# Kernel optimization log

Hardware: AMD Instinct MI355X
Metric: run time of the kernel (lower is better)

The kernel has to match this reference:

```python
import jax, jax.numpy as jnp
import numpy as np

T, B = 384, 128
IN_DIM, HID, OUT_DIM = 512, 1024, 512


def _lstm_step(h, c, x_t, Wx, Wh, b):
    # x_t: [B, D], h/c: [B, H]; gates order: i, f, g, o
    gates = x_t @ Wx + h @ Wh + b  # [B, 4H]
    i, f, g, o = jnp.split(gates, 4, axis=-1)
    c_new = jax.nn.sigmoid(f) * c + jax.nn.sigmoid(i) * jnp.tanh(g)
    h_new = jax.nn.sigmoid(o) * jnp.tanh(c_new)
    return h_new, c_new


def setup_inputs() -> dict:
    key = jax.random.key(0)
    ks = jax.random.split(key, 9)
    s_in = 1.0 / np.sqrt(IN_DIM)
    s_h = 1.0 / np.sqrt(HID)
    s_o = 1.0 / np.sqrt(OUT_DIM)
    return {
        "x": jax.random.normal(ks[0], (T, B, IN_DIM), dtype=jnp.float32),
        "hidden_state": jnp.zeros((1, B, HID), dtype=jnp.float32),
        "cell_state": jnp.zeros((1, B, HID), dtype=jnp.float32),
        "enc_Wx": jax.random.normal(ks[1], (IN_DIM, 4 * HID), dtype=jnp.float32) * s_in,
        "enc_Wh": jax.random.normal(ks[2], (HID, 4 * HID), dtype=jnp.float32) * s_h,
        "enc_b": jnp.zeros((4 * HID,), dtype=jnp.float32),
        "dec_Wx": jax.random.normal(ks[3], (OUT_DIM, 4 * HID), dtype=jnp.float32) * s_o,
        "dec_Wh": jax.random.normal(ks[4], (HID, 4 * HID), dtype=jnp.float32) * s_h,
        "dec_b": jnp.zeros((4 * HID,), dtype=jnp.float32),
        "fc_W": jax.random.normal(ks[5], (HID, OUT_DIM), dtype=jnp.float32) * s_h,
        "fc_b": jnp.zeros((OUT_DIM,), dtype=jnp.float32),
    }


def reference(x, hidden_state, cell_state, enc_Wx, enc_Wh, enc_b,
              dec_Wx, dec_Wh, dec_b, fc_W, fc_b):
    # ---- encoder: run LSTM over T steps, keep only final hidden state ----
    h0, c0 = hidden_state[0], cell_state[0]  # [B, H]

    def enc_step(carry, x_t):
        h, c = carry
        h, c = _lstm_step(h, c, x_t, enc_Wx, enc_Wh, enc_b)
        return (h, c), None

    (h_enc, _), _ = jax.lax.scan(enc_step, (h0, c0), x)

    y0 = jnp.zeros((B, OUT_DIM), dtype=x.dtype)
    c_dec0 = jnp.zeros((B, HID), dtype=x.dtype)

    def dec_step(carry, _):
        y, h, c = carry
        h, c = _lstm_step(h, c, y, dec_Wx, dec_Wh, dec_b)
        y = jax.nn.softmax(h @ fc_W + fc_b, axis=-1)  # softmax over dim=2
        return (y, h, c), y

    _, output = jax.lax.scan(dec_step, (y0, h_enc, c_dec0), None, length=T)
    return output  # [T, B, OUT_DIM]
```

## Files before the change

### kernel.cpp

```cpp
#include <hip/hip_runtime.h>


#define TS 384

typedef __attribute__((ext_vector_type(8))) short bf16x8;
typedef __attribute__((ext_vector_type(4))) float f32x4;

#define ACT_PLANE 393216u
#define WS_ACT 4096u
#define WS_FP  (WS_ACT + 4u*ACT_PLANE)
#define WS_TOTAL (WS_FP + 2097152u)

__device__ __forceinline__ unsigned short bf16r(float v) {
  unsigned u = __float_as_uint(v);
  u += 0x7FFFu + ((u >> 16) & 1u);
  return (unsigned short)(u >> 16);
}
__device__ __forceinline__ float bf2f(unsigned short h) {
  return __uint_as_float(((unsigned)h) << 16);
}
__device__ __forceinline__ void split2(float v, short& hi, short& lo) {
  unsigned short h = bf16r(v);
  float r = v - bf2f(h);
  hi = (short)h; lo = (short)bf16r(r);
}
__device__ __forceinline__ float sigm(float v)  { return 1.0f / (1.0f + __expf(-v)); }
__device__ __forceinline__ float tanhfa(float v){ return 1.0f - 2.0f / (__expf(2.0f*v) + 1.0f); }

__device__ __forceinline__ void st_u64(short* p, unsigned long long v) {
  __hip_atomic_store((unsigned long long*)p, v, __ATOMIC_RELAXED, __HIP_MEMORY_SCOPE_AGENT);
}
__device__ __forceinline__ void st_f32(float* p, float v) {
  __hip_atomic_store(p, v, __ATOMIC_RELAXED, __HIP_MEMORY_SCOPE_AGENT);
}
__device__ __forceinline__ float ld_f32(const float* p) {
  return __hip_atomic_load(p, __ATOMIC_RELAXED, __HIP_MEMORY_SCOPE_AGENT);
}
__device__ __forceinline__ unsigned ldc(const unsigned* p) {
  return __hip_atomic_load(p, __ATOMIC_RELAXED, __HIP_MEMORY_SCOPE_AGENT);
}

__device__ __forceinline__ int elem_off(int row, int k) {
  int kb = k >> 5, mt = row >> 4, lane = (((k >> 3) & 3) << 4) | (row & 15);
  return (((kb * 8 + mt) * 64) + lane) * 8 + (k & 7);
}

__device__ __forceinline__ void arrive(unsigned* line) {
  asm volatile("s_waitcnt vmcnt(0)" ::: "memory");
  __syncthreads();
  if (threadIdx.x == 0)
    __hip_atomic_fetch_add(line, 1u, __ATOMIC_RELAXED, __HIP_MEMORY_SCOPE_AGENT);
}
__device__ __forceinline__ void wait4(const unsigned* base, unsigned target,
                                      bool fence, int* sDead) {
  if (threadIdx.x == 0) {
    unsigned spins = 0;
    for (;;) {
      unsigned c0 = ldc(base), c1 = ldc(base + 64);
      unsigned c2 = ldc(base + 128), c3 = ldc(base + 192);
      if (c0 >= target && c1 >= target && c2 >= target && c3 >= target) break;
      __builtin_amdgcn_s_sleep(1);
      if (++spins > (1u << 19)) { *sDead = 1; break; }
    }
    if (fence) __builtin_amdgcn_fence(__ATOMIC_ACQUIRE, "agent");
  }
  __syncthreads();
}
__device__ __forceinline__ void wait1(const unsigned* line, unsigned target,
                                      bool fence, int* sDead) {
  if (threadIdx.x == 0) {
    unsigned spins = 0;
    while (ldc(line) < target) {
      __builtin_amdgcn_s_sleep(1);
      if (++spins > (1u << 19)) { *sDead = 1; break; }
    }
    if (fence) __builtin_amdgcn_fence(__ATOMIC_ACQUIRE, "agent");
  }
  __syncthreads();
}

__device__ void load_gate_weights(const float* __restrict__ Wx, const float* __restrict__ Wh,
                                  int p, short* sBh, short* sBl) {
  for (int idx = threadIdx.x; idx < 24576; idx += 1024) {
    int j = idx & 7, l = (idx >> 3) & 63, kb = idx >> 9;
    int k = kb * 32 + ((l >> 4) << 3) + j;
    int c = l & 15;
    int gcol = (c >> 2) * 1024 + p * 4 + (c & 3);
    float wv = (k < 512) ? Wx[(size_t)k * 4096 + gcol]
                         : Wh[(size_t)(k - 512) * 4096 + gcol];
    short hi, lo; split2(wv, hi, lo);
    sBh[idx] = hi; sBl[idx] = lo;
  }
}
__device__ void load_fc_weights(const float* __restrict__ fcW, int kg, int cg,
                                short* sFh, short* sFl) {
  for (int idx = threadIdx.x; idx < 4096; idx += 1024) {
    int j = idx & 7, l = (idx >> 3) & 63, kb = idx >> 9;
    int unit = kg * 256 + kb * 32 + ((l >> 4) << 3) + j;
    int col = cg * 16 + (l & 15);
    short hi, lo; split2(fcW[(size_t)unit * 512 + col], hi, lo);
    sFh[idx] = hi; sFl[idx] = lo;
  }
}

__device__ __forceinline__ void gg_range(
    const bf16x8* __restrict__ AH, const bf16x8* __restrict__ AL,
    const bf16x8* __restrict__ BH, const bf16x8* __restrict__ BL,
    int mt, int l, int kb0, int n2, f32x4* acc)
{
  #pragma unroll 2
  for (int i = 0; i < n2; ++i) {
    int kb = kb0 + i * 2;
    bf16x8 ah0 = AH[(kb * 8 + mt) * 64 + l];
    bf16x8 al0 = AL[(kb * 8 + mt) * 64 + l];
    bf16x8 bh0 = BH[kb * 64 + l];
    bf16x8 bl0 = BL[kb * 64 + l];
    bf16x8 ah1 = AH[((kb + 1) * 8 + mt) * 64 + l];
    bf16x8 al1 = AL[((kb + 1) * 8 + mt) * 64 + l];
    bf16x8 bh1 = BH[(kb + 1) * 64 + l];
    bf16x8 bl1 = BL[(kb + 1) * 64 + l];
    acc[0] = __builtin_amdgcn_mfma_f32_16x16x32_bf16(ah0, bh0, acc[0], 0, 0, 0);
    acc[1] = __builtin_amdgcn_mfma_f32_16x16x32_bf16(ah0, bl0, acc[1], 0, 0, 0);
    acc[2] = __builtin_amdgcn_mfma_f32_16x16x32_bf16(al0, bh0, acc[2], 0, 0, 0);
    acc[3] = __builtin_amdgcn_mfma_f32_16x16x32_bf16(ah1, bh1, acc[3], 0, 0, 0);
    acc[4] = __builtin_amdgcn_mfma_f32_16x16x32_bf16(ah1, bl1, acc[4], 0, 0, 0);
    acc[5] = __builtin_amdgcn_mfma_f32_16x16x32_bf16(al1, bh1, acc[5], 0, 0, 0);
  }
}
__device__ __forceinline__ void gg_finish(f32x4* acc, int kh, int mt, int l,
                                          float* LDSgate) {
  f32x4 s = (acc[0] + acc[3]) + ((acc[1] + acc[4]) + (acc[2] + acc[5]));
  const int col = l & 15, r0 = mt * 16 + ((l >> 4) << 2);
  float* plane = LDSgate + kh * 2176;
  #pragma unroll
  for (int j = 0; j < 4; ++j) plane[(r0 + j) * 17 + col] = s[j];
}

__device__ __forceinline__ void conv_x(const float* __restrict__ xsrc,
                                       short* dstH, short* dstL, int p, int t) {
  if (t < 32) {
    int g = p * 32 + t;
    int l = g & 63, mt = (g >> 6) & 7, kb = g >> 9;
    int row = mt * 16 + (l & 15), k = kb * 32 + ((l >> 4) << 3);
    const float* xs = xsrc + (size_t)row * 512 + k;
    unsigned long long h64[2] = {0, 0}, l64[2] = {0, 0};
    #pragma unroll
    for (int j = 0; j < 8; ++j) {
      short hi, lo; split2(xs[j], hi, lo);
      h64[j >> 2] |= (unsigned long long)(unsigned short)hi << ((j & 3) * 16);
      l64[j >> 2] |= (unsigned long long)(unsigned short)lo << ((j & 3) * 16);
    }
    int off = g * 8;
    st_u64(dstH + off, h64[0]); st_u64(dstH + off + 4, h64[1]);
    st_u64(dstL + off, l64[0]); st_u64(dstL + off + 4, l64[1]);
  }
}

__global__ void __launch_bounds__(1024, 1)
lstm3(const float* __restrict__ x, const float* __restrict__ h0p,
      const float* __restrict__ c0p, const float* __restrict__ eWx,
      const float* __restrict__ eWh, const float* __restrict__ eb,
      const float* __restrict__ dWx, const float* __restrict__ dWh,
      const float* __restrict__ db, const float* __restrict__ fcW,
      const float* __restrict__ fcb, float* __restrict__ out,
      char* __restrict__ ws)
{
  __shared__ __align__(16) short sBh[24576], sBl[24576];
  __shared__ __align__(16) short sFh[4096], sFl[4096];
  __shared__ float LDSgate[2 * 2176];
  __shared__ unsigned hsplit[512];
  __shared__ float ybuf[512];
  __shared__ float red[16];
  __shared__ int sDead;

  const int p = blockIdx.x, t = threadIdx.x;
  const int w = t >> 6, l = t & 63;
  const int mt = w & 7, kh = w >> 3;
  if (t == 0) sDead = 0;

  unsigned* hln = (unsigned*)ws;
  unsigned* yln = (unsigned*)(ws + 1024);
  unsigned* fln = (unsigned*)(ws + 2048);

  float* fp = (float*)(ws + WS_FP);
  short* planeH[2] = { (short*)(ws + WS_ACT),             (short*)(ws + WS_ACT + 2*ACT_PLANE) };
  short* planeL[2] = { (short*)(ws + WS_ACT + ACT_PLANE), (short*)(ws + WS_ACT + 3*ACT_PLANE) };

  const int row_pw = t & 127, u_pw = (t >> 7) & 3;
  unsigned* my_hline = hln + (p >> 6) * 64;

  load_gate_weights(eWx, eWh, p, sBh, sBl);
  conv_x(x, planeH[0], planeL[0], p, t);
  if (t < 64) {
    int g = 8192 + p * 64 + t;
    int ll = g & 63, mtt = (g >> 6) & 7, kb = g >> 9;
    int row = mtt * 16 + (ll & 15), k = kb * 32 + ((ll >> 4) << 3);
    const float* hs = h0p + (size_t)row * 1024 + (k - 512);
    unsigned long long h64[2] = {0, 0}, l64[2] = {0, 0};
    #pragma unroll
    for (int j = 0; j < 8; ++j) {
      short hi, lo; split2(hs[j], hi, lo);
      h64[j >> 2] |= (unsigned long long)(unsigned short)hi << ((j & 3) * 16);
      l64[j >> 2] |= (unsigned long long)(unsigned short)lo << ((j & 3) * 16);
    }
    int off = g * 8;
    st_u64(planeH[0] + off, h64[0]); st_u64(planeH[0] + off + 4, h64[1]);
    st_u64(planeL[0] + off, l64[0]); st_u64(planeL[0] + off + 4, l64[1]);
  }
  float creg = 0.f, bq0 = 0.f, bq1 = 0.f, bq2 = 0.f, bq3 = 0.f;
  if (t < 512) {
    creg = c0p[(size_t)row_pw * 1024 + p * 4 + u_pw];
    bq0 = eb[0 * 1024 + p * 4 + u_pw];
    bq1 = eb[1 * 1024 + p * 4 + u_pw];
    bq2 = eb[2 * 1024 + p * 4 + u_pw];
    bq3 = eb[3 * 1024 + p * 4 + u_pw];
  }
  arrive(my_hline);

  for (int st = 0; st < TS; ++st) {
    int rb = st & 1, wb = rb ^ 1;
    wait4(hln, 64u * (st + 1), true, &sDead);
    if (sDead) return;
    {
      f32x4 z = {0.f, 0.f, 0.f, 0.f};
      f32x4 acc[6] = {z, z, z, z, z, z};
      gg_range((const bf16x8*)planeH[rb], (const bf16x8*)planeL[rb],
               (const bf16x8*)sBh, (const bf16x8*)sBl, mt, l, kh * 24, 12, acc);
      gg_finish(acc, kh, mt, l, LDSgate);
    }
    __syncthreads();
    if (t < 512) {
      float g0 = LDSgate[row_pw * 17 + 0  + u_pw] + LDSgate[2176 + row_pw * 17 + 0  + u_pw] + bq0;
      float g1 = LDSgate[row_pw * 17 + 4  + u_pw] + LDSgate[2176 + row_pw * 17 + 4  + u_pw] + bq1;
      float g2 = LDSgate[row_pw * 17 + 8  + u_pw] + LDSgate[2176 + row_pw * 17 + 8  + u_pw] + bq2;
      float g3 = LDSgate[row_pw * 17 + 12 + u_pw] + LDSgate[2176 + row_pw * 17 + 12 + u_pw] + bq3;
      creg = sigm(g1) * creg + sigm(g0) * tanhfa(g2);
      float h = sigm(g3) * tanhfa(creg);
      short hi, lo; split2(h, hi, lo);
      hsplit[u_pw * 128 + row_pw] = ((unsigned)(unsigned short)hi << 16) | (unsigned short)lo;
    }
    if (st + 1 < TS) conv_x(x + (size_t)(st + 1) * 128 * 512, planeH[wb], planeL[wb], p, t);
    __syncthreads();
    if (t < 128) {
      int r = t;
      unsigned w0 = hsplit[r], w1 = hsplit[128 + r], w2 = hsplit[256 + r], w3 = hsplit[384 + r];
      unsigned long long hi64 = (unsigned long long)(w0 >> 16)
        | ((unsigned long long)(w1 >> 16) << 16)
        | ((unsigned long long)(w2 >> 16) << 32)
        | ((unsigned long long)(w3 >> 16) << 48);
      unsigned long long lo64 = (unsigned long long)(w0 & 0xFFFFu)
        | ((unsigned long long)(w1 & 0xFFFFu) << 16)
        | ((unsigned long long)(w2 & 0xFFFFu) << 32)
        | ((unsigned long long)(w3 & 0xFFFFu) << 48);
      int off = elem_off(r, 512 + p * 4);
      st_u64(planeH[wb] + off, hi64);
      st_u64(planeL[wb] + off, lo64);
    }
    arrive(my_hline);
  }

  load_gate_weights(dWx, dWh, p, sBh, sBl);
  if (p < 128) load_fc_weights(fcW, p >> 5, p & 31, sFh, sFl);
  if (t < 32) {
    int off = (p * 32 + t) * 8;
    st_u64(planeH[0] + off, 0ull); st_u64(planeH[0] + off + 4, 0ull);
    st_u64(planeL[0] + off, 0ull); st_u64(planeL[0] + off + 4, 0ull);
  }
  creg = 0.0f;
  if (t < 512) {
    bq0 = db[0 * 1024 + p * 4 + u_pw];
    bq1 = db[1 * 1024 + p * 4 + u_pw];
    bq2 = db[2 * 1024 + p * 4 + u_pw];
    bq3 = db[3 * 1024 + p * 4 + u_pw];
  }
  float fcb_r = (t < 512) ? fcb[t] : 0.f;
  arrive(my_hline);

  const unsigned HB = (unsigned)(TS + 2);
  for (int st = 0; st < TS; ++st) {
    int rb = st & 1, wb = rb ^ 1;
    f32x4 z = {0.f, 0.f, 0.f, 0.f};
    f32x4 acc[6] = {z, z, z, z, z, z};
    wait4(hln, 64u * (HB + st), true, &sDead);
    if (sDead) return;
    gg_range((const bf16x8*)planeH[rb], (const bf16x8*)planeL[rb],
             (const bf16x8*)sBh, (const bf16x8*)sBl, mt, l, 16 + kh * 16, 8, acc);
    wait4(yln, 32u * st, true, &sDead);
    if (sDead) return;
    gg_range((const bf16x8*)planeH[rb], (const bf16x8*)planeL[rb],
             (const bf16x8*)sBh, (const bf16x8*)sBl, mt, l, kh * 8, 4, acc);
    gg_finish(acc, kh, mt, l, LDSgate);
    __syncthreads();
    if (t < 512) {
      float g0 = LDSgate[row_pw * 17 + 0  + u_pw] + LDSgate[2176 + row_pw * 17 + 0  + u_pw] + bq0;
      float g1 = LDSgate[row_pw * 17 + 4  + u_pw] + LDSgate[2176 + row_pw * 17 + 4  + u_pw] + bq1;
      float g2 = LDSgate[row_pw * 17 + 8  + u_pw] + LDSgate[2176 + row_pw * 17 + 8  + u_pw] + bq2;
      float g3 = LDSgate[row_pw * 17 + 12 + u_pw] + LDSgate[2176 + row_pw * 17 + 12 + u_pw] + bq3;
      creg = sigm(g1) * creg + sigm(g0) * tanhfa(g2);
      float h = sigm(g3) * tanhfa(creg);
      short hi, lo; split2(h, hi, lo);
      hsplit[u_pw * 128 + row_pw] = ((unsigned)(unsigned short)hi << 16) | (unsigned short)lo;
    }
    __syncthreads();
    if (t < 128) {
      int r = t;
      unsigned w0 = hsplit[r], w1 = hsplit[128 + r], w2 = hsplit[256 + r], w3 = hsplit[384 + r];
      unsigned long long hi64 = (unsigned long long)(w0 >> 16)
        | ((unsigned long long)(w1 >> 16) << 16)
        | ((unsigned long long)(w2 >> 16) << 32)
        | ((unsigned long long)(w3 >> 16) << 48);
      unsigned long long lo64 = (unsigned long long)(w0 & 0xFFFFu)
        | ((unsigned long long)(w1 & 0xFFFFu) << 16)
        | ((unsigned long long)(w2 & 0xFFFFu) << 32)
        | ((unsigned long long)(w3 & 0xFFFFu) << 48);
      int off = elem_off(r, 512 + p * 4);
      st_u64(planeH[wb] + off, hi64);
      st_u64(planeL[wb] + off, lo64);
    }
    arrive(my_hline);
    if (p < 128) {
      const int kg = p >> 5, cg = p & 31;
      wait1(hln + kg * 64, 64u * (HB + st + 1), true, &sDead);
      if (sDead) return;
      {
        const bf16x8* AH = (const bf16x8*)planeH[wb];
        const bf16x8* AL = (const bf16x8*)planeL[wb];
        const bf16x8* BH = (const bf16x8*)sFh;
        const bf16x8* BL = (const bf16x8*)sFl;
        f32x4 a0 = z, a1 = z, a2 = z;
        #pragma unroll
        for (int kb = 0; kb < 4; ++kb) {
          int gkb = 16 + kg * 8 + kh * 4 + kb;
          bf16x8 ah = AH[(gkb * 8 + mt) * 64 + l];
          bf16x8 al = AL[(gkb * 8 + mt) * 64 + l];
          bf16x8 bh = BH[(kh * 4 + kb) * 64 + l];
          bf16x8 bl = BL[(kh * 4 + kb) * 64 + l];
          a0 = __builtin_amdgcn_mfma_f32_16x16x32_bf16(ah, bh, a0, 0, 0, 0);
          a1 = __builtin_amdgcn_mfma_f32_16x16x32_bf16(ah, bl, a1, 0, 0, 0);
          a2 = __builtin_amdgcn_mfma_f32_16x16x32_bf16(al, bh, a2, 0, 0, 0);
        }
        f32x4 s = a0 + (a1 + a2);
        int slice = kg * 2 + kh;
        int col = cg * 16 + (l & 15), r0 = mt * 16 + ((l >> 4) << 2);
        #pragma unroll
        for (int j = 0; j < 4; ++j)
          st_f32(&fp[(size_t)(slice * 128 + r0 + j) * 512 + col], s[j]);
      }
      arrive(fln + (p >> 5) * 64);
      wait4(fln, 32u * (st + 1), false, &sDead);
      if (sDead) return;
      float v = 0.f, e = 0.f, mx;
      if (t < 512) {
        v = fcb_r;
        #pragma unroll
        for (int s8 = 0; s8 < 8; ++s8)
          v += ld_f32(&fp[(size_t)(s8 * 128 + p) * 512 + t]);
        mx = v;
        #pragma unroll
        for (int o = 32; o > 0; o >>= 1) mx = fmaxf(mx, __shfl_xor(mx, o));
        if (l == 0) red[w] = mx;
      }
      __syncthreads();
      if (t < 512) {
        mx = red[0];
        #pragma unroll
        for (int i = 1; i < 8; ++i) mx = fmaxf(mx, red[i]);
        e = __expf(v - mx);
        float ss = e;
        #pragma unroll
        for (int o = 32; o > 0; o >>= 1) ss += __shfl_xor(ss, o);
        if (l == 0) red[8 + w] = ss;
      }
      __syncthreads();
      if (t < 512) {
        float ss = (red[8] + red[9]) + (red[10] + red[11])
                 + (red[12] + red[13]) + (red[14] + red[15]);
        float y = e / ss;
        out[((size_t)st * 128 + p) * 512 + t] = y;
        ybuf[t] = y;
      }
      __syncthreads();
      if (t < 64) {
        int kb = t >> 2, seg = t & 3;
        int k = kb * 32 + seg * 8;
        int lane_ = (seg << 4) | (p & 15), mtt = p >> 4;
        int off = ((kb * 8 + mtt) * 64 + lane_) * 8;
        unsigned long long h64[2] = {0, 0}, l64[2] = {0, 0};
        #pragma unroll
        for (int j = 0; j < 8; ++j) {
          short hi, lo; split2(ybuf[k + j], hi, lo);
          h64[j >> 2] |= (unsigned long long)(unsigned short)hi << ((j & 3) * 16);
          l64[j >> 2] |= (unsigned long long)(unsigned short)lo << ((j & 3) * 16);
        }
        st_u64(planeH[wb] + off, h64[0]); st_u64(planeH[wb] + off + 4, h64[1]);
        st_u64(planeL[wb] + off, l64[0]); st_u64(planeL[wb] + off + 4, l64[1]);
      }
      arrive(yln + (p >> 5) * 64);
    }
  }
}

extern "C" void kernel_launch(void* const* d_in, const int* in_sizes, int n_in,
                              void* d_out, int out_size, void* d_ws, size_t ws_size,
                              hipStream_t stream) {
  const float* x   = (const float*)d_in[0];
  const float* h0  = (const float*)d_in[1];
  const float* c0  = (const float*)d_in[2];
  const float* eWx = (const float*)d_in[3];
  const float* eWh = (const float*)d_in[4];
  const float* eb  = (const float*)d_in[5];
  const float* dWx = (const float*)d_in[6];
  const float* dWh = (const float*)d_in[7];
  const float* db  = (const float*)d_in[8];
  const float* fcW = (const float*)d_in[9];
  const float* fcb = (const float*)d_in[10];
  float* out = (float*)d_out;

  if (ws_size < (size_t)WS_TOTAL) {
    hipMemsetAsync(d_out, 0xFF, (size_t)out_size * sizeof(float), stream);
    return;
  }
  hipMemsetAsync(d_ws, 0, 4096, stream);
  hipLaunchKernelGGL(lstm3, dim3(256), dim3(1024), 0, stream,
                     x, h0, c0, eWx, eWh, eb, dWx, dWh, db, fcW, fcb, out,
                     (char*)d_ws);
}
```

Measured before the change: 16.87 ms.

## Split x and h activation planes to overlap input GEMM with barrier wait

The single combined activation plane is replaced by separate ring buffers: a 4-slot buffer for converted x / y inputs and a double buffer for h. In the encoder, the x-part of the gate GEMM now runs before waiting on the h barrier, and x conversion is prefetched two steps ahead. In the decoder, the FC projection moves to blocks 128-255 while softmax runs on blocks 0-127, and one acquire fence is dropped. This is meant to hide the per-step grid-barrier latency behind useful MFMA work, at the cost of more workspace and more complex synchronisation that relies on relaxed ordering.

New measurement: 14.97 ms. -11.3%, faster.

```diff
diff --git a/kernel.cpp b/kernel.cpp
--- a/kernel.cpp
+++ b/kernel.cpp
@@ -6,10 +6,12 @@
 typedef __attribute__((ext_vector_type(8))) short bf16x8;
 typedef __attribute__((ext_vector_type(4))) float f32x4;
 
-#define ACT_PLANE 393216u
-#define WS_ACT 4096u
-#define WS_FP  (WS_ACT + 4u*ACT_PLANE)
-#define WS_TOTAL (WS_FP + 2097152u)
+#define WS_XR 4096u
+#define XR_SLOT 262144u
+#define WS_HP (WS_XR + 4u*XR_SLOT)
+#define HP_BUF 524288u
+#define WS_FPN (WS_HP + 2u*HP_BUF)
+#define WS_TOTAL (WS_FPN + 2097152u)
 
 __device__ __forceinline__ unsigned short bf16r(float v) {
   unsigned u = __float_as_uint(v);
@@ -38,11 +40,6 @@
 }
 __device__ __forceinline__ unsigned ldc(const unsigned* p) {
   return __hip_atomic_load(p, __ATOMIC_RELAXED, __HIP_MEMORY_SCOPE_AGENT);
-}
-
-__device__ __forceinline__ int elem_off(int row, int k) {
-  int kb = k >> 5, mt = row >> 4, lane = (((k >> 3) & 3) << 4) | (row & 15);
-  return (((kb * 8 + mt) * 64) + lane) * 8 + (k & 7);
 }
 
 __device__ __forceinline__ void arrive(unsigned* line) {
@@ -67,14 +64,13 @@
   __syncthreads();
 }
 __device__ __forceinline__ void wait1(const unsigned* line, unsigned target,
-                                      bool fence, int* sDead) {
+                                      int* sDead) {
   if (threadIdx.x == 0) {
     unsigned spins = 0;
     while (ldc(line) < target) {
       __builtin_amdgcn_s_sleep(1);
       if (++spins > (1u << 19)) { *sDead = 1; break; }
     }
-    if (fence) __builtin_amdgcn_fence(__ATOMIC_ACQUIRE, "agent");
   }
   __syncthreads();
 }
@@ -103,20 +99,23 @@
   }
 }
 
-__device__ __forceinline__ void gg_range(
-    const bf16x8* __restrict__ AH, const bf16x8* __restrict__ AL,
-    const bf16x8* __restrict__ BH, const bf16x8* __restrict__ BL,
-    int mt, int l, int kb0, int n2, f32x4* acc)
+__device__ __forceinline__ void gg(const short* AHs, const short* ALs,
+    const short* BHs, const short* BLs, int mt, int l,
+    int kbA0, int kbB0, int nkb, f32x4* acc)
 {
+  const bf16x8* AH = (const bf16x8*)AHs;
+  const bf16x8* AL = (const bf16x8*)ALs;
+  const bf16x8* BH = (const bf16x8*)BHs;
+  const bf16x8* BL = (const bf16x8*)BLs;
   #pragma unroll 2
-  for (int i = 0; i < n2; ++i) {
-    int kb = kb0 + i * 2;
-    bf16x8 ah0 = AH[(kb * 8 + mt) * 64 + l];
-    bf16x8 al0 = AL[(kb * 8 + mt) * 64 + l];
+  for (int i = 0; i < nkb; i += 2) {
+    int ka = kbA0 + i, kb = kbB0 + i;
+    bf16x8 ah0 = AH[(ka * 8 + mt) * 64 + l];
+    bf16x8 al0 = AL[(ka * 8 + mt) * 64 + l];
     bf16x8 bh0 = BH[kb * 64 + l];
     bf16x8 bl0 = BL[kb * 64 + l];
-    bf16x8 ah1 = AH[((kb + 1) * 8 + mt) * 64 + l];
-    bf16x8 al1 = AL[((kb + 1) * 8 + mt) * 64 + l];
+    bf16x8 ah1 = AH[((ka + 1) * 8 + mt) * 64 + l];
+    bf16x8 al1 = AL[((ka + 1) * 8 + mt) * 64 + l];
     bf16x8 bh1 = BH[(kb + 1) * 64 + l];
     bf16x8 bl1 = BL[(kb + 1) * 64 + l];
     acc[0] = __builtin_amdgcn_mfma_f32_16x16x32_bf16(ah0, bh0, acc[0], 0, 0, 0);
@@ -157,7 +156,7 @@
 }
 
 __global__ void __launch_bounds__(1024, 1)
-lstm3(const float* __restrict__ x, const float* __restrict__ h0p,
+lstm4(const float* __restrict__ x, const float* __restrict__ h0p,
       const float* __restrict__ c0p, const float* __restrict__ eWx,
       const float* __restrict__ eWh, const float* __restrict__ eb,
       const float* __restrict__ dWx, const float* __restrict__ dWh,
@@ -181,21 +180,32 @@
   unsigned* hln = (unsigned*)ws;
   unsigned* yln = (unsigned*)(ws + 1024);
   unsigned* fln = (unsigned*)(ws + 2048);
-
-  float* fp = (float*)(ws + WS_FP);
-  short* planeH[2] = { (short*)(ws + WS_ACT),             (short*)(ws + WS_ACT + 2*ACT_PLANE) };
-  short* planeL[2] = { (short*)(ws + WS_ACT + ACT_PLANE), (short*)(ws + WS_ACT + 3*ACT_PLANE) };
+  unsigned* my_hline = hln + (p >> 6) * 64;
+
+  short* xrH[4]; short* xrL[4];
+  #pragma unroll
+  for (int s4 = 0; s4 < 4; ++s4) {
+    xrH[s4] = (short*)(ws + WS_XR + s4 * XR_SLOT);
+    xrL[s4] = (short*)(ws + WS_XR + s4 * XR_SLOT + 131072u);
+  }
+  short* hpH[2]; short* hpL[2];
+  #pragma unroll
+  for (int b2 = 0; b2 < 2; ++b2) {
+    hpH[b2] = (short*)(ws + WS_HP + b2 * HP_BUF);
+    hpL[b2] = (short*)(ws + WS_HP + b2 * HP_BUF + 262144u);
+  }
+  float* fp = (float*)(ws + WS_FPN);
 
   const int row_pw = t & 127, u_pw = (t >> 7) & 3;
-  unsigned* my_hline = hln + (p >> 6) * 64;
 
   load_gate_weights(eWx, eWh, p, sBh, sBl);
-  conv_x(x, planeH[0], planeL[0], p, t);
+  conv_x(x, xrH[0], xrL[0], p, t);
+  conv_x(x + 65536, xrH[1], xrL[1], p, t);
   if (t < 64) {
-    int g = 8192 + p * 64 + t;
-    int ll = g & 63, mtt = (g >> 6) & 7, kb = g >> 9;
-    int row = mtt * 16 + (ll & 15), k = kb * 32 + ((ll >> 4) << 3);
-    const float* hs = h0p + (size_t)row * 1024 + (k - 512);
+    int hg = p * 64 + t;
+    int ll = hg & 63, mtt = (hg >> 6) & 7, hk = hg >> 9;
+    int row = mtt * 16 + (ll & 15), k = hk * 32 + ((ll >> 4) << 3);
+    const float* hs = h0p + (size_t)row * 1024 + k;
     unsigned long long h64[2] = {0, 0}, l64[2] = {0, 0};
     #pragma unroll
     for (int j = 0; j < 8; ++j) {
@@ -203,9 +213,9 @@
       h64[j >> 2] |= (unsigned long long)(unsigned short)hi << ((j & 3) * 16);
       l64[j >> 2] |= (unsigned long long)(unsigned short)lo << ((j & 3) * 16);
     }
-    int off = g * 8;
-    st_u64(planeH[0] + off, h64[0]); st_u64(planeH[0] + off + 4, h64[1]);
-    st_u64(planeL[0] + off, l64[0]); st_u64(planeL[0] + off + 4, l64[1]);
+    int off = hg * 8;
+    st_u64(hpH[0] + off, h64[0]); st_u64(hpH[0] + off + 4, h64[1]);
+    st_u64(hpL[0] + off, l64[0]); st_u64(hpL[0] + off + 4, l64[1]);
   }
   float creg = 0.f, bq0 = 0.f, bq1 = 0.f, bq2 = 0.f, bq3 = 0.f;
   if (t < 512) {
@@ -216,18 +226,18 @@
     bq3 = eb[3 * 1024 + p * 4 + u_pw];
   }
   arrive(my_hline);
+  wait4(hln, 64u, true, &sDead);
+  if (sDead) return;
 
   for (int st = 0; st < TS; ++st) {
-    int rb = st & 1, wb = rb ^ 1;
+    int rb = st & 1, wb = rb ^ 1, xs = st & 3;
+    f32x4 z = {0.f, 0.f, 0.f, 0.f};
+    f32x4 acc[6] = {z, z, z, z, z, z};
+    gg(xrH[xs], xrL[xs], sBh, sBl, mt, l, kh * 8, kh * 8, 8, acc);
     wait4(hln, 64u * (st + 1), true, &sDead);
     if (sDead) return;
-    {
-      f32x4 z = {0.f, 0.f, 0.f, 0.f};
-      f32x4 acc[6] = {z, z, z, z, z, z};
-      gg_range((const bf16x8*)planeH[rb], (const bf16x8*)planeL[rb],
-               (const bf16x8*)sBh, (const bf16x8*)sBl, mt, l, kh * 24, 12, acc);
-      gg_finish(acc, kh, mt, l, LDSgate);
-    }
+    gg(hpH[rb], hpL[rb], sBh, sBl, mt, l, kh * 16, 16 + kh * 16, 16, acc);
+    gg_finish(acc, kh, mt, l, LDSgate);
     __syncthreads();
     if (t < 512) {
       float g0 = LDSgate[row_pw * 17 + 0  + u_pw] + LDSgate[2176 + row_pw * 17 + 0  + u_pw] + bq0;
@@ -239,7 +249,8 @@
       short hi, lo; split2(h, hi, lo);
       hsplit[u_pw * 128 + row_pw] = ((unsigned)(unsigned short)hi << 16) | (unsigned short)lo;
     }
-    if (st + 1 < TS) conv_x(x + (size_t)(st + 1) * 128 * 512, planeH[wb], planeL[wb], p, t);
+    if (st + 2 < TS)
+      conv_x(x + (size_t)(st + 2) * 65536, xrH[(st + 2) & 3], xrL[(st + 2) & 3], p, t);
     __syncthreads();
     if (t < 128) {
       int r = t;
@@ -252,19 +263,21 @@
         | ((unsigned long long)(w1 & 0xFFFFu) << 16)
         | ((unsigned long long)(w2 & 0xFFFFu) << 32)
         | ((unsigned long long)(w3 & 0xFFFFu) << 48);
-      int off = elem_off(r, 512 + p * 4);
-      st_u64(planeH[wb] + off, hi64);
-      st_u64(planeL[wb] + off, lo64);
+      int hk = p >> 3, mtt = r >> 4;
+      int lane_ = (((p >> 1) & 3) << 4) | (r & 15);
+      int off = ((hk * 8 + mtt) * 64 + lane_) * 8 + (p & 1) * 4;
+      st_u64(hpH[wb] + off, hi64);
+      st_u64(hpL[wb] + off, lo64);
     }
     arrive(my_hline);
   }
 
   load_gate_weights(dWx, dWh, p, sBh, sBl);
-  if (p < 128) load_fc_weights(fcW, p >> 5, p & 31, sFh, sFl);
+  if (p >= 128) load_fc_weights(fcW, (p - 128) >> 5, (p - 128) & 31, sFh, sFl);
   if (t < 32) {
     int off = (p * 32 + t) * 8;
-    st_u64(planeH[0] + off, 0ull); st_u64(planeH[0] + off + 4, 0ull);
-    st_u64(planeL[0] + off, 0ull); st_u64(planeL[0] + off + 4, 0ull);
+    st_u64(xrH[0] + off, 0ull); st_u64(xrH[0] + off + 4, 0ull);
+    st_u64(xrL[0] + off, 0ull); st_u64(xrL[0] + off + 4, 0ull);
   }
   creg = 0.0f;
   if (t < 512) {
@@ -279,16 +292,15 @@
   const unsigned HB = (unsigned)(TS + 2);
   for (int st = 0; st < TS; ++st) {
     int rb = st & 1, wb = rb ^ 1;
+    int ys = st & 1, yw = ys ^ 1;
     f32x4 z = {0.f, 0.f, 0.f, 0.f};
     f32x4 acc[6] = {z, z, z, z, z, z};
     wait4(hln, 64u * (HB + st), true, &sDead);
     if (sDead) return;
-    gg_range((const bf16x8*)planeH[rb], (const bf16x8*)planeL[rb],
-             (const bf16x8*)sBh, (const bf16x8*)sBl, mt, l, 16 + kh * 16, 8, acc);
-    wait4(yln, 32u * st, true, &sDead);
+    gg(hpH[rb], hpL[rb], sBh, sBl, mt, l, kh * 16, 16 + kh * 16, 16, acc);
+    wait4(yln, 32u * st, false, &sDead);
     if (sDead) return;
-    gg_range((const bf16x8*)planeH[rb], (const bf16x8*)planeL[rb],
-             (const bf16x8*)sBh, (const bf16x8*)sBl, mt, l, kh * 8, 4, acc);
+    gg(xrH[ys], xrL[ys], sBh, sBl, mt, l, kh * 8, kh * 8, 8, acc);
     gg_finish(acc, kh, mt, l, LDSgate);
     __syncthreads();
     if (t < 512) {
@@ -313,26 +325,29 @@
         | ((unsigned long long)(w1 & 0xFFFFu) << 16)
         | ((unsigned long long)(w2 & 0xFFFFu) << 32)
         | ((unsigned long long)(w3 & 0xFFFFu) << 48);
-      int off = elem_off(r, 512 + p * 4);
-      st_u64(planeH[wb] + off, hi64);
-      st_u64(planeL[wb] + off, lo64);
+      int hk = p >> 3, mtt = r >> 4;
+      int lane_ = (((p >> 1) & 3) << 4) | (r & 15);
+      int off = ((hk * 8 + mtt) * 64 + lane_) * 8 + (p & 1) * 4;
+      st_u64(hpH[wb] + off, hi64);
+      st_u64(hpL[wb] + off, lo64);
     }
     arrive(my_hline);
-    if (p < 128) {
-      const int kg = p >> 5, cg = p & 31;
-      wait1(hln + kg * 64, 64u * (HB + st + 1), true, &sDead);
+
+    if (p >= 128) {
+      const int f = p - 128, kg = f >> 5, cg = f & 31;
+      wait1(hln + kg * 64, 64u * (HB + st + 1), &sDead);
       if (sDead) return;
       {
-        const bf16x8* AH = (const bf16x8*)planeH[wb];
-        const bf16x8* AL = (const bf16x8*)planeL[wb];
+        const bf16x8* AH = (const bf16x8*)hpH[wb];
+        const bf16x8* AL = (const bf16x8*)hpL[wb];
         const bf16x8* BH = (const bf16x8*)sFh;
         const bf16x8* BL = (const bf16x8*)sFl;
         f32x4 a0 = z, a1 = z, a2 = z;
         #pragma unroll
         for (int kb = 0; kb < 4; ++kb) {
-          int gkb = 16 + kg * 8 + kh * 4 + kb;
-          bf16x8 ah = AH[(gkb * 8 + mt) * 64 + l];
-          bf16x8 al = AL[(gkb * 8 + mt) * 64 + l];
+          int hk = kg * 8 + kh * 4 + kb;
+          bf16x8 ah = AH[(hk * 8 + mt) * 64 + l];
+          bf16x8 al = AL[(hk * 8 + mt) * 64 + l];
           bf16x8 bh = BH[(kh * 4 + kb) * 64 + l];
           bf16x8 bl = BL[(kh * 4 + kb) * 64 + l];
           a0 = __builtin_amdgcn_mfma_f32_16x16x32_bf16(ah, bh, a0, 0, 0, 0);
@@ -346,7 +361,8 @@
         for (int j = 0; j < 4; ++j)
           st_f32(&fp[(size_t)(slice * 128 + r0 + j) * 512 + col], s[j]);
       }
-      arrive(fln + (p >> 5) * 64);
+      arrive(fln + (f >> 5) * 64);
+    } else {
       wait4(fln, 32u * (st + 1), false, &sDead);
       if (sDead) return;
       float v = 0.f, e = 0.f, mx;
@@ -392,8 +408,8 @@
           h64[j >> 2] |= (unsigned long long)(unsigned short)hi << ((j & 3) * 16);
           l64[j >> 2] |= (unsigned long long)(unsigned short)lo << ((j & 3) * 16);
         }
-        st_u64(planeH[wb] + off, h64[0]); st_u64(planeH[wb] + off + 4, h64[1]);
-        st_u64(planeL[wb] + off, l64[0]); st_u64(planeL[wb] + off + 4, l64[1]);
+        st_u64(xrH[yw] + off, h64[0]); st_u64(xrH[yw] + off + 4, h64[1]);
+        st_u64(xrL[yw] + off, l64[0]); st_u64(xrL[yw] + off + 4, l64[1]);
       }
       arrive(yln + (p >> 5) * 64);
     }
@@ -421,7 +437,7 @@
     return;
   }
   hipMemsetAsync(d_ws, 0, 4096, stream);
-  hipLaunchKernelGGL(lstm3, dim3(256), dim3(1024), 0, stream,
+  hipLaunchKernelGGL(lstm4, dim3(256), dim3(1024), 0, stream,
                      x, h0, c0, eWx, eWh, eb, dWx, dWh, db, fcW, fcb, out,
                      (char*)d_ws);
 }
```
